# Optimization experiments

Measured on AMD Instinct MI355X. Metric: run time of the kernel, lower is better.

Reference implementation:

```python
import jax, jax.numpy as jnp
import numpy as np

HIDDEN = 1024
VOCAB = 50257
MAX_LEN = 12


def setup_inputs() -> dict:
    key = jax.random.key(0)
    ks = jax.random.split(key, 16)
    H, V, L = HIDDEN, VOCAB, MAX_LEN
    s = 1.0 / np.sqrt(H)
    inp = {
        "input": jax.random.randint(ks[0], (1, 1), 0, V, dtype=jnp.int64),
        "h_hidden": jax.random.normal(ks[1], (1, 1, H), dtype=jnp.float32),
        "c_hidden": jax.random.normal(ks[2], (1, 1, H), dtype=jnp.float32),
        "encoder_outputs": jax.random.normal(ks[3], (L, H), dtype=jnp.float32),
        # parameters (PyTorch layout: Linear weight is [out, in])
        "emb": jax.random.normal(ks[4], (V, H), dtype=jnp.float32),
        "attn_W": jax.random.uniform(ks[5], (L, 2 * H), jnp.float32, -s, s),
        "attn_b": jax.random.uniform(ks[6], (L,), jnp.float32, -s, s),
        "comb_W": jax.random.uniform(ks[7], (H, 2 * H), jnp.float32, -s, s),
        "comb_b": jax.random.uniform(ks[8], (H,), jnp.float32, -s, s),
        "W_ih": jax.random.uniform(ks[9], (4 * H, H), jnp.float32, -s, s),
        "W_hh": jax.random.uniform(ks[10], (4 * H, H), jnp.float32, -s, s),
        "b_ih": jax.random.uniform(ks[11], (4 * H,), jnp.float32, -s, s),
        "b_hh": jax.random.uniform(ks[12], (4 * H,), jnp.float32, -s, s),
        "out_W": jax.random.uniform(ks[13], (V, H), jnp.float32, -s, s),
        "out_b": jax.random.uniform(ks[14], (V,), jnp.float32, -s, s),
    }
    return inp


def reference(input, h_hidden, c_hidden, encoder_outputs, emb, attn_W, attn_b,
              comb_W, comb_b, W_ih, W_hh, b_ih, b_hh, out_W, out_b):
    H = HIDDEN
    # embedding lookup -> [1, H] (dropout is identity in eval mode)
    embedded = emb[input.reshape(-1)].reshape(1, H)
    h0 = h_hidden[0]  # [1, H]
    c0 = c_hidden[0]  # [1, H]
    # attention weights over MAX_LEN encoder positions
    attn_in = jnp.concatenate([embedded, h0], axis=1)            # [1, 2H]
    attn_weights = jax.nn.softmax(attn_in @ attn_W.T + attn_b, axis=1)  # [1, 12]
    attn_applied = attn_weights @ encoder_outputs                # [1, H]
    # combine + relu
    x = jnp.concatenate([embedded, attn_applied], axis=1)        # [1, 2H]
    x = jax.nn.relu(x @ comb_W.T + comb_b)                       # [1, H]
    # single LSTM cell step (gate order i, f, g, o as in PyTorch)
    gates = x @ W_ih.T + b_ih + h0 @ W_hh.T + b_hh               # [1, 4H]
    i, f, g, o = jnp.split(gates, 4, axis=1)
    i, f, o = jax.nn.sigmoid(i), jax.nn.sigmoid(f), jax.nn.sigmoid(o)
    c_new = f * c0 + i * jnp.tanh(g)
    h_new = o * jnp.tanh(c_new)
    # output projection + log-softmax over vocab
    logp = jax.nn.log_softmax(h_new @ out_W.T + out_b, axis=1)   # [1, V]
    return (logp, (h_new[None], c_new[None]), attn_weights)
```

## Files before the change

### kernel.cpp

```cpp
#include <hip/hip_runtime.h>
#include <math.h>

#define HID 1024
#define VOC 50257
#define MLEN 12

__device__ __forceinline__ float wave_reduce_sum(float v) {
    for (int off = 32; off > 0; off >>= 1)
        v += __shfl_down(v, off, 64);
    return v;
}

__global__ __launch_bounds__(256) void k1_embed_attn(
    const int* __restrict__ tok_p, const float* __restrict__ h0,
    const float* __restrict__ enc, const float* __restrict__ emb,
    const float* __restrict__ attn_W, const float* __restrict__ attn_b,
    float* __restrict__ ws_xin, float* __restrict__ out_attnw)
{
    __shared__ float lds_logits[MLEN];
    __shared__ float lds_w[MLEN];
    const int t = threadIdx.x;
    const int wid = t >> 6, lane = t & 63;
    const int tok = tok_p[0];
    const float4* emb4 = (const float4*)(emb + (size_t)tok * HID);
    const float4* h04  = (const float4*)h0;
    const float4* aW4  = (const float4*)attn_W;

    for (int l = wid; l < MLEN; l += 4) {
        float s = 0.f;
        for (int k = 0; k < 8; ++k) {
            int idx = k * 64 + lane;
            float4 v = (idx < 256) ? emb4[idx] : h04[idx - 256];
            float4 w = aW4[l * 512 + idx];
            s += v.x * w.x + v.y * w.y + v.z * w.z + v.w * w.w;
        }
        s = wave_reduce_sum(s);
        if (lane == 0) lds_logits[l] = s + attn_b[l];
    }
    __syncthreads();
    if (t == 0) {
        float m = -1e30f;
        for (int l = 0; l < MLEN; ++l) m = fmaxf(m, lds_logits[l]);
        float ssum = 0.f;
        for (int l = 0; l < MLEN; ++l) { float e = expf(lds_logits[l] - m); lds_w[l] = e; ssum += e; }
        float inv = 1.f / ssum;
        for (int l = 0; l < MLEN; ++l) { lds_w[l] *= inv; out_attnw[l] = lds_w[l]; }
    }
    __syncthreads();

    const float4* enc4 = (const float4*)enc;
    float4 e = emb4[t];
    float4 acc = make_float4(0.f, 0.f, 0.f, 0.f);
    for (int l = 0; l < MLEN; ++l) {
        float wl = lds_w[l];
        float4 v = enc4[l * 256 + t];
        acc.x += wl * v.x; acc.y += wl * v.y; acc.z += wl * v.z; acc.w += wl * v.w;
    }
    float4* xin4 = (float4*)ws_xin;
    xin4[t] = e;
    xin4[256 + t] = acc;
}

__global__ __launch_bounds__(256) void k2_comb(
    const float* __restrict__ ws_xin, const float* __restrict__ comb_W,
    const float* __restrict__ comb_b, float* __restrict__ ws_x)
{
    const int wid = threadIdx.x >> 6, lane = threadIdx.x & 63;
    const int row = blockIdx.x * 4 + wid;
    const float4* W4 = (const float4*)(comb_W + (size_t)row * 2048);
    const float4* v4 = (const float4*)ws_xin;
    float s = 0.f;
    for (int k = 0; k < 8; ++k) {
        int idx = k * 64 + lane;
        float4 w = W4[idx], v = v4[idx];
        s += w.x * v.x + w.y * v.y + w.z * v.z + w.w * v.w;
    }
    s = wave_reduce_sum(s);
    if (lane == 0) ws_x[row] = fmaxf(s + comb_b[row], 0.f);
}

__global__ __launch_bounds__(256) void k3_gates(
    const float* __restrict__ ws_x, const float* __restrict__ h0,
    const float* __restrict__ W_ih, const float* __restrict__ W_hh,
    const float* __restrict__ b_ih, const float* __restrict__ b_hh,
    float* __restrict__ ws_gates)
{
    const int wid = threadIdx.x >> 6, lane = threadIdx.x & 63;
    const int row = blockIdx.x * 4 + wid;
    const float4* Wi4 = (const float4*)(W_ih + (size_t)row * HID);
    const float4* Wh4 = (const float4*)(W_hh + (size_t)row * HID);
    const float4* x4  = (const float4*)ws_x;
    const float4* h4  = (const float4*)h0;
    float s = 0.f;
    for (int k = 0; k < 4; ++k) {
        int idx = k * 64 + lane;
        float4 wi = Wi4[idx], xv = x4[idx];
        float4 wh = Wh4[idx], hv = h4[idx];
        s += wi.x * xv.x + wi.y * xv.y + wi.z * xv.z + wi.w * xv.w;
        s += wh.x * hv.x + wh.y * hv.y + wh.z * hv.z + wh.w * hv.w;
    }
    s = wave_reduce_sum(s);
    if (lane == 0) ws_gates[row] = s + b_ih[row] + b_hh[row];
}

__global__ __launch_bounds__(1024) void k4_lstm(
    const float* __restrict__ ws_gates, const float* __restrict__ c0,
    float* __restrict__ out_h, float* __restrict__ out_c, float* __restrict__ ws_h)
{
    const int t = threadIdx.x;
    float ig = ws_gates[t];
    float fg = ws_gates[HID + t];
    float gg = ws_gates[2 * HID + t];
    float og = ws_gates[3 * HID + t];
    float i = 1.f / (1.f + expf(-ig));
    float f = 1.f / (1.f + expf(-fg));
    float o = 1.f / (1.f + expf(-og));
    float g = tanhf(gg);
    float c = f * c0[t] + i * g;
    float h = o * tanhf(c);
    out_c[t] = c;
    out_h[t] = h;
    ws_h[t] = h;
}

__global__ __launch_bounds__(256) void k5_logits(
    const float* __restrict__ ws_h, const float* __restrict__ out_W,
    const float* __restrict__ out_b, float* __restrict__ out_logp)
{
    const int wid = threadIdx.x >> 6, lane = threadIdx.x & 63;
    const int row = blockIdx.x * 4 + wid;
    if (row >= VOC) return;
    const float4* W4 = (const float4*)(out_W + (size_t)row * HID);
    const float4* h4 = (const float4*)ws_h;
    float s = 0.f;
    for (int k = 0; k < 4; ++k) {
        int idx = k * 64 + lane;
        float4 w = W4[idx], h = h4[idx];
        s += w.x * h.x + w.y * h.y + w.z * h.z + w.w * h.w;
    }
    s = wave_reduce_sum(s);
    if (lane == 0) out_logp[row] = s + out_b[row];
}

__global__ __launch_bounds__(1024) void k6_lse(
    const float* __restrict__ logits, float* __restrict__ ws_lse)
{
    __shared__ float red[16];
    __shared__ float red2[16];
    const int t = threadIdx.x;
    const int wid = t >> 6, lane = t & 63;
    float m = -1e30f;
    for (int i = t; i < VOC; i += 1024) m = fmaxf(m, logits[i]);
    for (int off = 32; off > 0; off >>= 1) m = fmaxf(m, __shfl_xor(m, off, 64));
    if (lane == 0) red[wid] = m;
    __syncthreads();
    if (t == 0) {
        float mm = red[0];
        for (int w = 1; w < 16; ++w) mm = fmaxf(mm, red[w]);
        red[0] = mm;
    }
    __syncthreads();
    m = red[0];
    float s = 0.f;
    for (int i = t; i < VOC; i += 1024) s += expf(logits[i] - m);
    s = wave_reduce_sum(s);
    if (lane == 0) red2[wid] = s;
    __syncthreads();
    if (t == 0) {
        float ss = 0.f;
        for (int w = 0; w < 16; ++w) ss += red2[w];
        ws_lse[0] = m + logf(ss);
    }
}

__global__ __launch_bounds__(256) void k7_sub(
    float* __restrict__ out_logp, const float* __restrict__ ws_lse)
{
    const int i = blockIdx.x * 256 + threadIdx.x;
    if (i < VOC) out_logp[i] -= ws_lse[0];
}

extern "C" void kernel_launch(void* const* d_in, const int* in_sizes, int n_in,
                              void* d_out, int out_size, void* d_ws, size_t ws_size,
                              hipStream_t stream) {
    const int*   tok      = (const int*)d_in[0];
    const float* h_hidden = (const float*)d_in[1];
    const float* c_hidden = (const float*)d_in[2];
    const float* enc      = (const float*)d_in[3];
    const float* emb      = (const float*)d_in[4];
    const float* attn_W   = (const float*)d_in[5];
    const float* attn_b   = (const float*)d_in[6];
    const float* comb_W   = (const float*)d_in[7];
    const float* comb_b   = (const float*)d_in[8];
    const float* W_ih     = (const float*)d_in[9];
    const float* W_hh     = (const float*)d_in[10];
    const float* b_ih     = (const float*)d_in[11];
    const float* b_hh     = (const float*)d_in[12];
    const float* out_W    = (const float*)d_in[13];
    const float* out_b    = (const float*)d_in[14];

    float* out       = (float*)d_out;
    float* out_logp  = out;
    float* out_h     = out + VOC;
    float* out_c     = out + VOC + HID;
    float* out_attnw = out + VOC + 2 * HID;

    float* ws       = (float*)d_ws;
    float* ws_xin   = ws;
    float* ws_x     = ws + 2048;
    float* ws_gates = ws + 3072;
    float* ws_h     = ws + 7168;
    float* ws_lse   = ws + 8192;

    k1_embed_attn<<<1, 256, 0, stream>>>(tok, h_hidden, enc, emb, attn_W, attn_b,
                                         ws_xin, out_attnw);
    k2_comb<<<HID / 4, 256, 0, stream>>>(ws_xin, comb_W, comb_b, ws_x);
    k3_gates<<<4 * HID / 4, 256, 0, stream>>>(ws_x, h_hidden, W_ih, W_hh, b_ih, b_hh, ws_gates);
    k4_lstm<<<1, 1024, 0, stream>>>(ws_gates, c_hidden, out_h, out_c, ws_h);
    k5_logits<<<(VOC + 3) / 4, 256, 0, stream>>>(ws_h, out_W, out_b, out_logp);
    k6_lse<<<1, 1024, 0, stream>>>(out_logp, ws_lse);
    k7_sub<<<(VOC + 255) / 256, 256, 0, stream>>>(out_logp, ws_lse);
}
```

Baseline: 439.0 us.

## Hoist input-independent matvecs into first kernel and fuse LSTM via last-block atomic

The first kernel now runs attention in one block while other blocks compute the embedding half of the combine layer and the W_hh·h0 gate term. A further set of blocks touches the start of out_W to warm the cache. The combine kernel then only handles the attention half. The gate kernel finishes the LSTM elementwise step in the last-arriving block, found through an atomic counter. This removes a launch and moves independent work off the serial path, at the cost of a grid-wide atomic and extra cache-warming traffic.

Result: slower. 453.9 us (+3.4%).

```diff
diff --git a/kernel.cpp b/kernel.cpp
--- a/kernel.cpp
+++ b/kernel.cpp
@@ -4,6 +4,19 @@
 #define HID 1024
 #define VOC 50257
 #define MLEN 12
+
+#define K1_DOT_BLOCKS 1280
+#define K1_PREF_BLOCKS 128
+#define PREF_F4 32
+
+#define WS_ATTN   0
+#define WS_X      1024
+#define WS_PCOMB  2048
+#define WS_HH     3072
+#define WS_GATES  7168
+#define WS_H      11264
+#define WS_LSE    12288
+#define WS_CTR    12292
 
 __device__ __forceinline__ float wave_reduce_sum(float v) {
     for (int off = 32; off > 0; off >>= 1)
@@ -11,127 +24,164 @@
     return v;
 }
 
-__global__ __launch_bounds__(256) void k1_embed_attn(
+__global__ __launch_bounds__(256) void k1_fused(
     const int* __restrict__ tok_p, const float* __restrict__ h0,
     const float* __restrict__ enc, const float* __restrict__ emb,
     const float* __restrict__ attn_W, const float* __restrict__ attn_b,
-    float* __restrict__ ws_xin, float* __restrict__ out_attnw)
-{
-    __shared__ float lds_logits[MLEN];
-    __shared__ float lds_w[MLEN];
+    const float* __restrict__ comb_W, const float* __restrict__ comb_b,
+    const float* __restrict__ W_hh, const float* __restrict__ b_ih,
+    const float* __restrict__ b_hh, const float* __restrict__ out_W,
+    float* __restrict__ ws, float* __restrict__ out_attnw)
+{
     const int t = threadIdx.x;
     const int wid = t >> 6, lane = t & 63;
+    const int bid = blockIdx.x;
     const int tok = tok_p[0];
     const float4* emb4 = (const float4*)(emb + (size_t)tok * HID);
     const float4* h04  = (const float4*)h0;
-    const float4* aW4  = (const float4*)attn_W;
-
-    for (int l = wid; l < MLEN; l += 4) {
+
+    if (bid == 0) {
+        __shared__ float lds_logits[MLEN];
+        __shared__ float lds_w[MLEN];
+        if (t == 0) *((unsigned int*)(ws + WS_CTR)) = 0u;
+        const float4* aW4 = (const float4*)attn_W;
+        for (int l = wid; l < MLEN; l += 4) {
+            float s = 0.f;
+            for (int k = 0; k < 8; ++k) {
+                int idx = k * 64 + lane;
+                float4 v = (idx < 256) ? emb4[idx] : h04[idx - 256];
+                float4 w = aW4[l * 512 + idx];
+                s += v.x * w.x + v.y * w.y + v.z * w.z + v.w * w.w;
+            }
+            s = wave_reduce_sum(s);
+            if (lane == 0) lds_logits[l] = s + attn_b[l];
+        }
+        __syncthreads();
+        if (t == 0) {
+            float m = -1e30f;
+            for (int l = 0; l < MLEN; ++l) m = fmaxf(m, lds_logits[l]);
+            float ssum = 0.f;
+            for (int l = 0; l < MLEN; ++l) { float e = expf(lds_logits[l] - m); lds_w[l] = e; ssum += e; }
+            float inv = 1.f / ssum;
+            for (int l = 0; l < MLEN; ++l) { lds_w[l] *= inv; out_attnw[l] = lds_w[l]; }
+        }
+        __syncthreads();
+        const float4* enc4 = (const float4*)enc;
+        float4 acc = make_float4(0.f, 0.f, 0.f, 0.f);
+        for (int l = 0; l < MLEN; ++l) {
+            float wl = lds_w[l];
+            float4 v = enc4[l * 256 + t];
+            acc.x += wl * v.x; acc.y += wl * v.y; acc.z += wl * v.z; acc.w += wl * v.w;
+        }
+        ((float4*)(ws + WS_ATTN))[t] = acc;
+    } else if (bid <= K1_DOT_BLOCKS) {
+        const int gw = (bid - 1) * 4 + wid;
         float s = 0.f;
-        for (int k = 0; k < 8; ++k) {
-            int idx = k * 64 + lane;
-            float4 v = (idx < 256) ? emb4[idx] : h04[idx - 256];
-            float4 w = aW4[l * 512 + idx];
-            s += v.x * w.x + v.y * w.y + v.z * w.z + v.w * w.w;
-        }
-        s = wave_reduce_sum(s);
-        if (lane == 0) lds_logits[l] = s + attn_b[l];
-    }
-    __syncthreads();
-    if (t == 0) {
-        float m = -1e30f;
-        for (int l = 0; l < MLEN; ++l) m = fmaxf(m, lds_logits[l]);
-        float ssum = 0.f;
-        for (int l = 0; l < MLEN; ++l) { float e = expf(lds_logits[l] - m); lds_w[l] = e; ssum += e; }
-        float inv = 1.f / ssum;
-        for (int l = 0; l < MLEN; ++l) { lds_w[l] *= inv; out_attnw[l] = lds_w[l]; }
-    }
-    __syncthreads();
-
-    const float4* enc4 = (const float4*)enc;
-    float4 e = emb4[t];
-    float4 acc = make_float4(0.f, 0.f, 0.f, 0.f);
-    for (int l = 0; l < MLEN; ++l) {
-        float wl = lds_w[l];
-        float4 v = enc4[l * 256 + t];
-        acc.x += wl * v.x; acc.y += wl * v.y; acc.z += wl * v.z; acc.w += wl * v.w;
-    }
-    float4* xin4 = (float4*)ws_xin;
-    xin4[t] = e;
-    xin4[256 + t] = acc;
+        if (gw < HID) {
+            const float4* W4 = (const float4*)(comb_W + (size_t)gw * 2 * HID);
+            for (int k = 0; k < 4; ++k) {
+                int idx = k * 64 + lane;
+                float4 w = W4[idx], v = emb4[idx];
+                s += w.x * v.x + w.y * v.y + w.z * v.z + w.w * v.w;
+            }
+            s = wave_reduce_sum(s);
+            if (lane == 0) ws[WS_PCOMB + gw] = s + comb_b[gw];
+        } else {
+            const int r = gw - HID;
+            const float4* W4 = (const float4*)(W_hh + (size_t)r * HID);
+            for (int k = 0; k < 4; ++k) {
+                int idx = k * 64 + lane;
+                float4 w = W4[idx], v = h04[idx];
+                s += w.x * v.x + w.y * v.y + w.z * v.z + w.w * v.w;
+            }
+            s = wave_reduce_sum(s);
+            if (lane == 0) ws[WS_HH + r] = s + b_ih[r] + b_hh[r];
+        }
+    } else {
+        const int pb = bid - K1_DOT_BLOCKS - 1;
+        const float4* W4 = (const float4*)out_W;
+        const int base = pb * 256 + t;
+        float acc = 0.f;
+        for (int i = 0; i < PREF_F4; ++i) {
+            float4 v = W4[base + i * (K1_PREF_BLOCKS * 256)];
+            acc += v.x + v.y + v.z + v.w;
+        }
+        asm volatile("" :: "v"(acc));
+    }
 }
 
 __global__ __launch_bounds__(256) void k2_comb(
-    const float* __restrict__ ws_xin, const float* __restrict__ comb_W,
-    const float* __restrict__ comb_b, float* __restrict__ ws_x)
+    const float* __restrict__ comb_W, float* __restrict__ ws)
 {
     const int wid = threadIdx.x >> 6, lane = threadIdx.x & 63;
     const int row = blockIdx.x * 4 + wid;
-    const float4* W4 = (const float4*)(comb_W + (size_t)row * 2048);
-    const float4* v4 = (const float4*)ws_xin;
-    float s = 0.f;
-    for (int k = 0; k < 8; ++k) {
+    const float4* W4 = (const float4*)(comb_W + (size_t)row * 2 * HID + HID);
+    const float4* v4 = (const float4*)(ws + WS_ATTN);
+    float s = 0.f;
+    for (int k = 0; k < 4; ++k) {
         int idx = k * 64 + lane;
         float4 w = W4[idx], v = v4[idx];
         s += w.x * v.x + w.y * v.y + w.z * v.z + w.w * v.w;
     }
     s = wave_reduce_sum(s);
-    if (lane == 0) ws_x[row] = fmaxf(s + comb_b[row], 0.f);
-}
-
-__global__ __launch_bounds__(256) void k3_gates(
-    const float* __restrict__ ws_x, const float* __restrict__ h0,
-    const float* __restrict__ W_ih, const float* __restrict__ W_hh,
-    const float* __restrict__ b_ih, const float* __restrict__ b_hh,
-    float* __restrict__ ws_gates)
+    if (lane == 0) ws[WS_X + row] = fmaxf(s + ws[WS_PCOMB + row], 0.f);
+}
+
+__global__ __launch_bounds__(256) void k3_gates_lstm(
+    const float* __restrict__ W_ih, const float* __restrict__ c0,
+    float* __restrict__ ws, float* __restrict__ out_h, float* __restrict__ out_c)
 {
     const int wid = threadIdx.x >> 6, lane = threadIdx.x & 63;
     const int row = blockIdx.x * 4 + wid;
-    const float4* Wi4 = (const float4*)(W_ih + (size_t)row * HID);
-    const float4* Wh4 = (const float4*)(W_hh + (size_t)row * HID);
-    const float4* x4  = (const float4*)ws_x;
-    const float4* h4  = (const float4*)h0;
+    const float4* W4 = (const float4*)(W_ih + (size_t)row * HID);
+    const float4* x4 = (const float4*)(ws + WS_X);
     float s = 0.f;
     for (int k = 0; k < 4; ++k) {
         int idx = k * 64 + lane;
-        float4 wi = Wi4[idx], xv = x4[idx];
-        float4 wh = Wh4[idx], hv = h4[idx];
-        s += wi.x * xv.x + wi.y * xv.y + wi.z * xv.z + wi.w * xv.w;
-        s += wh.x * hv.x + wh.y * hv.y + wh.z * hv.z + wh.w * hv.w;
-    }
-    s = wave_reduce_sum(s);
-    if (lane == 0) ws_gates[row] = s + b_ih[row] + b_hh[row];
-}
-
-__global__ __launch_bounds__(1024) void k4_lstm(
-    const float* __restrict__ ws_gates, const float* __restrict__ c0,
-    float* __restrict__ out_h, float* __restrict__ out_c, float* __restrict__ ws_h)
-{
-    const int t = threadIdx.x;
-    float ig = ws_gates[t];
-    float fg = ws_gates[HID + t];
-    float gg = ws_gates[2 * HID + t];
-    float og = ws_gates[3 * HID + t];
-    float i = 1.f / (1.f + expf(-ig));
-    float f = 1.f / (1.f + expf(-fg));
-    float o = 1.f / (1.f + expf(-og));
-    float g = tanhf(gg);
-    float c = f * c0[t] + i * g;
-    float h = o * tanhf(c);
-    out_c[t] = c;
-    out_h[t] = h;
-    ws_h[t] = h;
+        float4 w = W4[idx], v = x4[idx];
+        s += w.x * v.x + w.y * v.y + w.z * v.z + w.w * v.w;
+    }
+    s = wave_reduce_sum(s);
+    if (lane == 0) ws[WS_GATES + row] = s + ws[WS_HH + row];
+
+    __shared__ unsigned int lastflag;
+    __syncthreads();
+    if (threadIdx.x == 0) {
+        __threadfence();
+        unsigned int prev = atomicAdd((unsigned int*)(ws + WS_CTR), 1u);
+        lastflag = (prev == gridDim.x - 1) ? 1u : 0u;
+    }
+    __syncthreads();
+    if (lastflag) {
+        __threadfence();
+        const float* g = ws + WS_GATES;
+        for (int e = threadIdx.x; e < HID; e += 256) {
+            float ig = g[e];
+            float fg = g[HID + e];
+            float gg = g[2 * HID + e];
+            float og = g[3 * HID + e];
+            float i = 1.f / (1.f + expf(-ig));
+            float f = 1.f / (1.f + expf(-fg));
+            float o = 1.f / (1.f + expf(-og));
+            float gv = tanhf(gg);
+            float c = f * c0[e] + i * gv;
+            float h = o * tanhf(c);
+            out_c[e] = c;
+            out_h[e] = h;
+            ws[WS_H + e] = h;
+        }
+    }
 }
 
 __global__ __launch_bounds__(256) void k5_logits(
-    const float* __restrict__ ws_h, const float* __restrict__ out_W,
+    const float* __restrict__ ws, const float* __restrict__ out_W,
     const float* __restrict__ out_b, float* __restrict__ out_logp)
 {
     const int wid = threadIdx.x >> 6, lane = threadIdx.x & 63;
     const int row = blockIdx.x * 4 + wid;
     if (row >= VOC) return;
     const float4* W4 = (const float4*)(out_W + (size_t)row * HID);
-    const float4* h4 = (const float4*)ws_h;
+    const float4* h4 = (const float4*)(ws + WS_H);
     float s = 0.f;
     for (int k = 0; k < 4; ++k) {
         int idx = k * 64 + lane;
@@ -143,7 +193,7 @@
 }
 
 __global__ __launch_bounds__(1024) void k6_lse(
-    const float* __restrict__ logits, float* __restrict__ ws_lse)
+    const float* __restrict__ logits, float* __restrict__ ws)
 {
     __shared__ float red[16];
     __shared__ float red2[16];
@@ -169,15 +219,15 @@
     if (t == 0) {
         float ss = 0.f;
         for (int w = 0; w < 16; ++w) ss += red2[w];
-        ws_lse[0] = m + logf(ss);
+        ws[WS_LSE] = m + logf(ss);
     }
 }
 
 __global__ __launch_bounds__(256) void k7_sub(
-    float* __restrict__ out_logp, const float* __restrict__ ws_lse)
+    float* __restrict__ out_logp, const float* __restrict__ ws)
 {
     const int i = blockIdx.x * 256 + threadIdx.x;
-    if (i < VOC) out_logp[i] -= ws_lse[0];
+    if (i < VOC) out_logp[i] -= ws[WS_LSE];
 }
 
 extern "C" void kernel_launch(void* const* d_in, const int* in_sizes, int n_in,
@@ -205,19 +255,14 @@
     float* out_c     = out + VOC + HID;
     float* out_attnw = out + VOC + 2 * HID;
 
-    float* ws       = (float*)d_ws;
-    float* ws_xin   = ws;
-    float* ws_x     = ws + 2048;
-    float* ws_gates = ws + 3072;
-    float* ws_h     = ws + 7168;
-    float* ws_lse   = ws + 8192;
-
-    k1_embed_attn<<<1, 256, 0, stream>>>(tok, h_hidden, enc, emb, attn_W, attn_b,
-                                         ws_xin, out_attnw);
-    k2_comb<<<HID / 4, 256, 0, stream>>>(ws_xin, comb_W, comb_b, ws_x);
-    k3_gates<<<4 * HID / 4, 256, 0, stream>>>(ws_x, h_hidden, W_ih, W_hh, b_ih, b_hh, ws_gates);
-    k4_lstm<<<1, 1024, 0, stream>>>(ws_gates, c_hidden, out_h, out_c, ws_h);
-    k5_logits<<<(VOC + 3) / 4, 256, 0, stream>>>(ws_h, out_W, out_b, out_logp);
-    k6_lse<<<1, 1024, 0, stream>>>(out_logp, ws_lse);
-    k7_sub<<<(VOC + 255) / 256, 256, 0, stream>>>(out_logp, ws_lse);
-}
+    float* ws = (float*)d_ws;
+
+    k1_fused<<<1 + K1_DOT_BLOCKS + K1_PREF_BLOCKS, 256, 0, stream>>>(
+        tok, h_hidden, enc, emb, attn_W, attn_b, comb_W, comb_b,
+        W_hh, b_ih, b_hh, out_W, ws, out_attnw);
+    k2_comb<<<HID / 4, 256, 0, stream>>>(comb_W, ws);
+    k3_gates_lstm<<<4 * HID / 4, 256, 0, stream>>>(W_ih, c_hidden, ws, out_h, out_c);
+    k5_logits<<<(VOC + 3) / 4, 256, 0, stream>>>(ws, out_W, out_b, out_logp);
+    k6_lse<<<1, 1024, 0, stream>>>(out_logp, ws);
+    k7_sub<<<(VOC + 255) / 256, 256, 0, stream>>>(out_logp, ws);
+}
```

## Fuse decoder step into one cooperative persistent kernel with grid syncs

Applied to the files above, without the earlier changes.

Replaces the seven-kernel chain with a single cooperative kernel of 1024 blocks that separates the stages with grid.sync. The h0-dependent half of each matmul (the embedding part of comb and the W_hh gates) now runs alongside the attention computation. Idle blocks prefetch out_W into cache during the small stages. An online max/sum-exp is fused into the logits pass so the separate log-sum-exp kernel goes away. This removes launch overhead and serial gaps, at the cost of grid-wide barrier latency and a dependence on cooperative launch support, with the old kernels kept as a fallback.

Result: slower. 976.6 us (+122.5%).

```diff
diff --git a/kernel.cpp b/kernel.cpp
--- a/kernel.cpp
+++ b/kernel.cpp
@@ -1,14 +1,240 @@
 #include <hip/hip_runtime.h>
+#include <hip/hip_cooperative_groups.h>
 #include <math.h>
+
+namespace cg = cooperative_groups;
 
 #define HID 1024
 #define VOC 50257
 #define MLEN 12
+#define NB 1024
+#define NT 256
+
+#define WS_ATTN   0
+#define WS_X      1024
+#define WS_PCOMB  2048
+#define WS_HH     3072
+#define WS_GATES  7168
+#define WS_H      11264
+#define WS_PART   12288
 
 __device__ __forceinline__ float wave_reduce_sum(float v) {
     for (int off = 32; off > 0; off >>= 1)
         v += __shfl_down(v, off, 64);
     return v;
+}
+
+__device__ __forceinline__ void merge_ms(float& m, float& s, float m2, float s2) {
+    float M = fmaxf(m, m2);
+    s = s * expf(m - M) + s2 * expf(m2 - M);
+    m = M;
+}
+
+__global__ __launch_bounds__(NT, 4) void mega(
+    const int* __restrict__ tok_p, const float* __restrict__ h0,
+    const float* __restrict__ enc, const float* __restrict__ emb,
+    const float* __restrict__ attn_W, const float* __restrict__ attn_b,
+    const float* __restrict__ comb_W, const float* __restrict__ comb_b,
+    const float* __restrict__ W_ih, const float* __restrict__ W_hh,
+    const float* __restrict__ b_ih, const float* __restrict__ b_hh,
+    const float* __restrict__ out_W, const float* __restrict__ out_b,
+    const float* __restrict__ c0, float* __restrict__ ws,
+    float* __restrict__ out_logp, float* __restrict__ out_h,
+    float* __restrict__ out_c, float* __restrict__ out_attnw)
+{
+    cg::grid_group grid = cg::this_grid();
+    const int t = threadIdx.x;
+    const int wid = t >> 6, lane = t & 63;
+    const int bid = blockIdx.x;
+    __shared__ float lds_w[MLEN];
+    __shared__ float lds_m[4], lds_s[4];
+    __shared__ float lds_bcast;
+
+    const int tok = tok_p[0];
+    const float4* emb4 = (const float4*)(emb + (size_t)tok * HID);
+    const float4* h04  = (const float4*)h0;
+
+    if (bid == 0) {
+        __shared__ float lds_logits[MLEN];
+        const float4* aW4 = (const float4*)attn_W;
+        for (int l = wid; l < MLEN; l += 4) {
+            float s = 0.f;
+            for (int k = 0; k < 8; ++k) {
+                int idx = k * 64 + lane;
+                float4 v = (idx < 256) ? emb4[idx] : h04[idx - 256];
+                float4 w = aW4[l * 512 + idx];
+                s += v.x * w.x + v.y * w.y + v.z * w.z + v.w * w.w;
+            }
+            s = wave_reduce_sum(s);
+            if (lane == 0) lds_logits[l] = s + attn_b[l];
+        }
+        __syncthreads();
+        if (t == 0) {
+            float m = -1e30f;
+            for (int l = 0; l < MLEN; ++l) m = fmaxf(m, lds_logits[l]);
+            float ssum = 0.f;
+            for (int l = 0; l < MLEN; ++l) { float e = expf(lds_logits[l] - m); lds_w[l] = e; ssum += e; }
+            float inv = 1.f / ssum;
+            for (int l = 0; l < MLEN; ++l) { lds_w[l] *= inv; out_attnw[l] = lds_w[l]; }
+        }
+        __syncthreads();
+        const float4* enc4 = (const float4*)enc;
+        float4 acc = make_float4(0.f, 0.f, 0.f, 0.f);
+        for (int l = 0; l < MLEN; ++l) {
+            float wl = lds_w[l];
+            float4 v = enc4[l * 256 + t];
+            acc.x += wl * v.x; acc.y += wl * v.y; acc.z += wl * v.z; acc.w += wl * v.w;
+        }
+        ((float4*)(ws + WS_ATTN))[t] = acc;
+    } else {
+        const int gid = (bid - 1) * 4 + wid;
+        for (int task = gid; task < 5120; task += 4092) {
+            float s = 0.f;
+            if (task < 1024) {
+                const float4* W4 = (const float4*)(comb_W + (size_t)task * 2 * HID);
+                for (int k = 0; k < 4; ++k) {
+                    int idx = k * 64 + lane;
+                    float4 w = W4[idx], v = emb4[idx];
+                    s += w.x * v.x + w.y * v.y + w.z * v.z + w.w * v.w;
+                }
+                s = wave_reduce_sum(s);
+                if (lane == 0) ws[WS_PCOMB + task] = s + comb_b[task];
+            } else {
+                const int r = task - 1024;
+                const float4* W4 = (const float4*)(W_hh + (size_t)r * HID);
+                for (int k = 0; k < 4; ++k) {
+                    int idx = k * 64 + lane;
+                    float4 w = W4[idx], v = h04[idx];
+                    s += w.x * v.x + w.y * v.y + w.z * v.z + w.w * v.w;
+                }
+                s = wave_reduce_sum(s);
+                if (lane == 0) ws[WS_HH + r] = s + b_ih[r] + b_hh[r];
+            }
+        }
+    }
+    grid.sync();
+
+    {
+        const int gid = bid * 4 + wid;
+        if (gid < 1024) {
+            const float4* W4 = (const float4*)(comb_W + (size_t)gid * 2 * HID + HID);
+            const float4* v4 = (const float4*)(ws + WS_ATTN);
+            float s = 0.f;
+            for (int k = 0; k < 4; ++k) {
+                int idx = k * 64 + lane;
+                float4 w = W4[idx], v = v4[idx];
+                s += w.x * v.x + w.y * v.y + w.z * v.z + w.w * v.w;
+            }
+            s = wave_reduce_sum(s);
+            if (lane == 0) ws[WS_X + gid] = fmaxf(s + ws[WS_PCOMB + gid], 0.f);
+        } else if (bid >= 256 && bid < 512) {
+            const int p = bid - 256;
+            const float4* W4 = (const float4*)out_W;
+            float acc = 0.f;
+            for (int i = 0; i < 8; ++i) {
+                float4 v = W4[(size_t)p * 2048 + i * 256 + t];
+                acc += v.x + v.y + v.z + v.w;
+            }
+            asm volatile("" :: "v"(acc));
+        }
+    }
+    grid.sync();
+
+    {
+        const int r = bid * 4 + wid;
+        const float4* W4 = (const float4*)(W_ih + (size_t)r * HID);
+        const float4* x4 = (const float4*)(ws + WS_X);
+        float s = 0.f;
+        for (int k = 0; k < 4; ++k) {
+            int idx = k * 64 + lane;
+            float4 w = W4[idx], v = x4[idx];
+            s += w.x * v.x + w.y * v.y + w.z * v.z + w.w * v.w;
+        }
+        s = wave_reduce_sum(s);
+        if (lane == 0) ws[WS_GATES + r] = s + ws[WS_HH + r];
+    }
+    grid.sync();
+
+    if (bid == 0) {
+        const float* g = ws + WS_GATES;
+        for (int e = t; e < HID; e += NT) {
+            float i = 1.f / (1.f + expf(-g[e]));
+            float f = 1.f / (1.f + expf(-g[HID + e]));
+            float o = 1.f / (1.f + expf(-g[3 * HID + e]));
+            float gv = tanhf(g[2 * HID + e]);
+            float c = f * c0[e] + i * gv;
+            float h = o * tanhf(c);
+            out_c[e] = c;
+            out_h[e] = h;
+            ws[WS_H + e] = h;
+        }
+    } else if (bid >= 512) {
+        const int p = bid - 512;
+        const float4* W4 = (const float4*)out_W;
+        float acc = 0.f;
+        for (int i = 0; i < 8; ++i) {
+            float4 v = W4[524288 + (size_t)p * 2048 + i * 256 + t];
+            acc += v.x + v.y + v.z + v.w;
+        }
+        asm volatile("" :: "v"(acc));
+    }
+    grid.sync();
+
+    {
+        const float4* h4 = (const float4*)(ws + WS_H);
+        float4 hv[4];
+        #pragma unroll
+        for (int k = 0; k < 4; ++k) hv[k] = h4[k * 64 + lane];
+        const int gid = bid * 4 + wid;
+        float m = -1e30f, sacc = 0.f;
+        for (int r = gid; r < VOC; r += 4096) {
+            const float4* W4 = (const float4*)(out_W + (size_t)r * HID);
+            float s = 0.f;
+            #pragma unroll
+            for (int k = 0; k < 4; ++k) {
+                float4 w = W4[k * 64 + lane];
+                s += w.x * hv[k].x + w.y * hv[k].y + w.z * hv[k].z + w.w * hv[k].w;
+            }
+            s = wave_reduce_sum(s);
+            if (lane == 0) {
+                float v = s + out_b[r];
+                out_logp[r] = v;
+                if (v > m) { sacc = sacc * expf(m - v) + 1.f; m = v; }
+                else       { sacc += expf(v - m); }
+            }
+        }
+        if (lane == 0) { lds_m[wid] = m; lds_s[wid] = sacc; }
+        __syncthreads();
+        if (t == 0) {
+            float M = lds_m[0], S = lds_s[0];
+            for (int w = 1; w < 4; ++w) merge_ms(M, S, lds_m[w], lds_s[w]);
+            ws[WS_PART + 2 * bid]     = M;
+            ws[WS_PART + 2 * bid + 1] = S;
+        }
+    }
+    grid.sync();
+
+    {
+        float m = -1e30f, s = 0.f;
+        for (int p = t; p < NB; p += NT)
+            merge_ms(m, s, ws[WS_PART + 2 * p], ws[WS_PART + 2 * p + 1]);
+        for (int off = 32; off > 0; off >>= 1) {
+            float m2 = __shfl_xor(m, off, 64);
+            float s2 = __shfl_xor(s, off, 64);
+            merge_ms(m, s, m2, s2);
+        }
+        if (lane == 0) { lds_m[wid] = m; lds_s[wid] = s; }
+        __syncthreads();
+        if (t == 0) {
+            float M = lds_m[0], S = lds_s[0];
+            for (int w = 1; w < 4; ++w) merge_ms(M, S, lds_m[w], lds_s[w]);
+            lds_bcast = M + logf(S);
+        }
+        __syncthreads();
+        const float lse = lds_bcast;
+        const int i = bid * NT + t;
+        if (i < VOC) out_logp[i] -= lse;
+    }
 }
 
 __global__ __launch_bounds__(256) void k1_embed_attn(
@@ -25,7 +251,6 @@
     const float4* emb4 = (const float4*)(emb + (size_t)tok * HID);
     const float4* h04  = (const float4*)h0;
     const float4* aW4  = (const float4*)attn_W;
-
     for (int l = wid; l < MLEN; l += 4) {
         float s = 0.f;
         for (int k = 0; k < 8; ++k) {
@@ -47,7 +272,6 @@
         for (int l = 0; l < MLEN; ++l) { lds_w[l] *= inv; out_attnw[l] = lds_w[l]; }
     }
     __syncthreads();
-
     const float4* enc4 = (const float4*)enc;
     float4 e = emb4[t];
     float4 acc = make_float4(0.f, 0.f, 0.f, 0.f);
@@ -61,7 +285,7 @@
     xin4[256 + t] = acc;
 }
 
-__global__ __launch_bounds__(256) void k2_comb(
+__global__ __launch_bounds__(256) void k2_comb_fb(
     const float* __restrict__ ws_xin, const float* __restrict__ comb_W,
     const float* __restrict__ comb_b, float* __restrict__ ws_x)
 {
@@ -79,7 +303,7 @@
     if (lane == 0) ws_x[row] = fmaxf(s + comb_b[row], 0.f);
 }
 
-__global__ __launch_bounds__(256) void k3_gates(
+__global__ __launch_bounds__(256) void k3_gates_fb(
     const float* __restrict__ ws_x, const float* __restrict__ h0,
     const float* __restrict__ W_ih, const float* __restrict__ W_hh,
     const float* __restrict__ b_ih, const float* __restrict__ b_hh,
@@ -103,27 +327,21 @@
     if (lane == 0) ws_gates[row] = s + b_ih[row] + b_hh[row];
 }
 
-__global__ __launch_bounds__(1024) void k4_lstm(
+__global__ __launch_bounds__(1024) void k4_lstm_fb(
     const float* __restrict__ ws_gates, const float* __restrict__ c0,
     float* __restrict__ out_h, float* __restrict__ out_c, float* __restrict__ ws_h)
 {
     const int t = threadIdx.x;
-    float ig = ws_gates[t];
-    float fg = ws_gates[HID + t];
-    float gg = ws_gates[2 * HID + t];
-    float og = ws_gates[3 * HID + t];
-    float i = 1.f / (1.f + expf(-ig));
-    float f = 1.f / (1.f + expf(-fg));
-    float o = 1.f / (1.f + expf(-og));
-    float g = tanhf(gg);
+    float i = 1.f / (1.f + expf(-ws_gates[t]));
+    float f = 1.f / (1.f + expf(-ws_gates[HID + t]));
+    float o = 1.f / (1.f + expf(-ws_gates[3 * HID + t]));
+    float g = tanhf(ws_gates[2 * HID + t]);
     float c = f * c0[t] + i * g;
     float h = o * tanhf(c);
-    out_c[t] = c;
-    out_h[t] = h;
-    ws_h[t] = h;
-}
-
-__global__ __launch_bounds__(256) void k5_logits(
+    out_c[t] = c; out_h[t] = h; ws_h[t] = h;
+}
+
+__global__ __launch_bounds__(256) void k5_logits_fb(
     const float* __restrict__ ws_h, const float* __restrict__ out_W,
     const float* __restrict__ out_b, float* __restrict__ out_logp)
 {
@@ -142,7 +360,7 @@
     if (lane == 0) out_logp[row] = s + out_b[row];
 }
 
-__global__ __launch_bounds__(1024) void k6_lse(
+__global__ __launch_bounds__(1024) void k6_lse_fb(
     const float* __restrict__ logits, float* __restrict__ ws_lse)
 {
     __shared__ float red[16];
@@ -173,7 +391,7 @@
     }
 }
 
-__global__ __launch_bounds__(256) void k7_sub(
+__global__ __launch_bounds__(256) void k7_sub_fb(
     float* __restrict__ out_logp, const float* __restrict__ ws_lse)
 {
     const int i = blockIdx.x * 256 + threadIdx.x;
@@ -205,19 +423,31 @@
     float* out_c     = out + VOC + HID;
     float* out_attnw = out + VOC + 2 * HID;
 
-    float* ws       = (float*)d_ws;
-    float* ws_xin   = ws;
-    float* ws_x     = ws + 2048;
-    float* ws_gates = ws + 3072;
-    float* ws_h     = ws + 7168;
-    float* ws_lse   = ws + 8192;
-
-    k1_embed_attn<<<1, 256, 0, stream>>>(tok, h_hidden, enc, emb, attn_W, attn_b,
-                                         ws_xin, out_attnw);
-    k2_comb<<<HID / 4, 256, 0, stream>>>(ws_xin, comb_W, comb_b, ws_x);
-    k3_gates<<<4 * HID / 4, 256, 0, stream>>>(ws_x, h_hidden, W_ih, W_hh, b_ih, b_hh, ws_gates);
-    k4_lstm<<<1, 1024, 0, stream>>>(ws_gates, c_hidden, out_h, out_c, ws_h);
-    k5_logits<<<(VOC + 3) / 4, 256, 0, stream>>>(ws_h, out_W, out_b, out_logp);
-    k6_lse<<<1, 1024, 0, stream>>>(out_logp, ws_lse);
-    k7_sub<<<(VOC + 255) / 256, 256, 0, stream>>>(out_logp, ws_lse);
-}
+    float* ws = (float*)d_ws;
+
+    void* args[] = {
+        (void*)&tok, (void*)&h_hidden, (void*)&enc, (void*)&emb,
+        (void*)&attn_W, (void*)&attn_b, (void*)&comb_W, (void*)&comb_b,
+        (void*)&W_ih, (void*)&W_hh, (void*)&b_ih, (void*)&b_hh,
+        (void*)&out_W, (void*)&out_b, (void*)&c_hidden, (void*)&ws,
+        (void*)&out_logp, (void*)&out_h, (void*)&out_c, (void*)&out_attnw
+    };
+    hipError_t err = hipLaunchCooperativeKernel((const void*)mega, dim3(NB), dim3(NT),
+                                                args, 0, stream);
+    if (err != hipSuccess) {
+        float* ws_xin   = ws;
+        float* ws_x     = ws + 2048;
+        float* ws_gates = ws + 3072;
+        float* ws_h     = ws + 7168;
+        float* ws_lse   = ws + 8192;
+        k1_embed_attn<<<1, 256, 0, stream>>>(tok, h_hidden, enc, emb, attn_W, attn_b,
+                                             ws_xin, out_attnw);
+        k2_comb_fb<<<HID / 4, 256, 0, stream>>>(ws_xin, comb_W, comb_b, ws_x);
+        k3_gates_fb<<<4 * HID / 4, 256, 0, stream>>>(ws_x, h_hidden, W_ih, W_hh,
+                                                     b_ih, b_hh, ws_gates);
+        k4_lstm_fb<<<1, 1024, 0, stream>>>(ws_gates, c_hidden, out_h, out_c, ws_h);
+        k5_logits_fb<<<(VOC + 3) / 4, 256, 0, stream>>>(ws_h, out_W, out_b, out_logp);
+        k6_lse_fb<<<1, 1024, 0, stream>>>(out_logp, ws_lse);
+        k7_sub_fb<<<(VOC + 255) / 256, 256, 0, stream>>>(out_logp, ws_lse);
+    }
+}
```
